# Kernel optimization log

Measured on AMD Instinct MI355X. Metric: run time of the kernel, lower is better.

The kernel has to match this reference:

```python
import jax, jax.numpy as jnp
import numpy as np


def setup_inputs() -> dict:
    key = jax.random.key(0)
    k1, k2 = jax.random.split(key)
    B, N, S, C = 8, 65536, 4, 8
    psi = jax.random.normal(k1, (B, N, S), dtype=jnp.float32)
    # nn.Parameter(torch.randn(d_coord, d_spinor, d_spinor) / sqrt(d_spinor))
    gamma = jax.random.normal(k2, (C, S, S), dtype=jnp.float32) / jnp.sqrt(jnp.float32(S))
    return {"psi": psi, "gamma": gamma}


def reference(psi, gamma):
    # G[mu,nu] = gamma[mu] @ gamma[nu]  -> [C, C, S, S]
    G = jnp.einsum('mij,njk->mnik', gamma, gamma)
    Gt = jnp.swapaxes(G, 0, 1)                 # G[nu,mu]
    A = 0.5 * (G - Gt)                         # 0.5 * commutator  (K1 generator)
    Ssym = 0.5 * (G + Gt)                      # 0.5 * anticommutator (K2 generator)

    # K0: sigma = psi_bar psi (psi_bar == psi here)
    K0 = jnp.einsum('bni,bni->bn', psi, psi)   # [B, N]

    # Precompute small outer product per token, then contract once per output.
    outer = jnp.einsum('bni,bnj->bnij', psi, psi)   # [B, N, S, S] (small S=4)
    K1 = jnp.einsum('bnij,mnuv->bnmn'.replace('nu', 'x'), outer, A) if False else \
         jnp.einsum('bnij,cdij->bncd', outer, A)    # [B, N, C, C] antisymmetric
    K2 = jnp.einsum('bnij,cdij->bncd', outer, Ssym) # [B, N, C, C] symmetric
    return (K0, K1, K2)
```

## Files before the change

kernel.cpp:

```cpp
#include <hip/hip_runtime.h>


#define TPB 128
#define LDS_STRIDE 68

__device__ __forceinline__ float dot4(float4 a, float4 b) {
    return a.x * b.x + a.y * b.y + a.z * b.z + a.w * b.w;
}

__global__ __launch_bounds__(TPB) void spinor_bilinears_kernel(
    const float* __restrict__ psi,
    const float* __restrict__ gamma,
    float* __restrict__ out,
    long long n_tokens) {
    __shared__ float ldsT[TPB * LDS_STRIDE];

    const int tid = threadIdx.x;
    const long long t_glob = (long long)blockIdx.x * TPB + tid;

    float* K0 = out;
    float* K1 = out + n_tokens;
    float* K2 = out + n_tokens + n_tokens * 64;

    const float4 p = ((const float4*)psi)[t_glob];

    K0[t_glob] = dot4(p, p);

    float4 u[8], v[8];
    const float4* g4 = (const float4*)gamma;
#pragma unroll
    for (int c = 0; c < 8; ++c) {
        const float4 g0 = g4[c * 4 + 0];
        const float4 g1 = g4[c * 4 + 1];
        const float4 g2 = g4[c * 4 + 2];
        const float4 g3 = g4[c * 4 + 3];
        float4 uc;
        uc.x = p.x * g0.x + p.y * g1.x + p.z * g2.x + p.w * g3.x;
        uc.y = p.x * g0.y + p.y * g1.y + p.z * g2.y + p.w * g3.y;
        uc.z = p.x * g0.z + p.y * g1.z + p.z * g2.z + p.w * g3.z;
        uc.w = p.x * g0.w + p.y * g1.w + p.z * g2.w + p.w * g3.w;
        u[c] = uc;
        float4 vc;
        vc.x = dot4(g0, p);
        vc.y = dot4(g1, p);
        vc.z = dot4(g2, p);
        vc.w = dot4(g3, p);
        v[c] = vc;
    }

    float* row = &ldsT[tid * LDS_STRIDE];
#pragma unroll
    for (int c = 0; c < 8; ++c) {
        float4 t0, t1;
        t0.x = dot4(u[c], v[0]);
        t0.y = dot4(u[c], v[1]);
        t0.z = dot4(u[c], v[2]);
        t0.w = dot4(u[c], v[3]);
        t1.x = dot4(u[c], v[4]);
        t1.y = dot4(u[c], v[5]);
        t1.z = dot4(u[c], v[6]);
        t1.w = dot4(u[c], v[7]);
        ((float4*)(row + c * 8))[0] = t0;
        ((float4*)(row + c * 8))[1] = t1;
    }

    __syncthreads();

    const long long blk_base = (long long)blockIdx.x * (TPB * 64);
    float4* K1v = (float4*)(K1 + blk_base);
    float4* K2v = (float4*)(K2 + blk_base);

    const int cd0 = (tid & 15) * 4;
    const int c = cd0 >> 3;
    const int d0 = cd0 & 7;

#pragma unroll
    for (int it = 0; it < 16; ++it) {
        const int t = it * 8 + (tid >> 4);
        const float* trow = &ldsT[t * LDS_STRIDE];
        const float4 tcd = *(const float4*)(trow + cd0);
        const float td0 = trow[(d0 + 0) * 8 + c];
        const float td1 = trow[(d0 + 1) * 8 + c];
        const float td2 = trow[(d0 + 2) * 8 + c];
        const float td3 = trow[(d0 + 3) * 8 + c];

        float4 k1v, k2v;
        k1v.x = 0.5f * (tcd.x - td0);  k2v.x = 0.5f * (tcd.x + td0);
        k1v.y = 0.5f * (tcd.y - td1);  k2v.y = 0.5f * (tcd.y + td1);
        k1v.z = 0.5f * (tcd.z - td2);  k2v.z = 0.5f * (tcd.z + td2);
        k1v.w = 0.5f * (tcd.w - td3);  k2v.w = 0.5f * (tcd.w + td3);

        K1v[it * 128 + tid] = k1v;
        K2v[it * 128 + tid] = k2v;
    }
}

extern "C" void kernel_launch(void* const* d_in, const int* in_sizes, int n_in,
                              void* d_out, int out_size, void* d_ws, size_t ws_size,
                              hipStream_t stream) {
    const float* psi = (const float*)d_in[0];
    const float* gamma = (const float*)d_in[1];
    float* out = (float*)d_out;

    const long long n_tokens = (long long)in_sizes[0] / 4;
    const int blocks = (int)(n_tokens / TPB);

    spinor_bilinears_kernel<<<blocks, TPB, 0, stream>>>(psi, gamma, out, n_tokens);
}
```

Before: 269.6 us.

## Assign sixteen threads per token and compute outputs directly without LDS transpose

Replaces the one-thread-per-token kernel, which staged a 64-entry matrix per token through LDS, with a kernel where 16 threads cooperate on a token. Each thread computes one float4 of K1 and K2 directly, recomputing the transposed term instead of reading it from shared memory. This removes the large LDS allocation and barrier, raising occupancy and giving coalesced vector stores, now issued as nontemporal writes. The cost is redundant per-thread arithmetic and repeated gamma loads.

```diff
diff --git a/kernel.cpp b/kernel.cpp
--- a/kernel.cpp
+++ b/kernel.cpp
@@ -1,98 +1,84 @@
 #include <hip/hip_runtime.h>
 
 
-#define TPB 128
-#define LDS_STRIDE 68
+#define TPB 256
+
+typedef float f32x4 __attribute__((ext_vector_type(4)));
 
 __device__ __forceinline__ float dot4(float4 a, float4 b) {
     return a.x * b.x + a.y * b.y + a.z * b.z + a.w * b.w;
 }
 
-__global__ __launch_bounds__(TPB) void spinor_bilinears_kernel(
+__global__ __launch_bounds__(TPB) void spinor_bilinears_direct(
     const float* __restrict__ psi,
     const float* __restrict__ gamma,
     float* __restrict__ out,
     long long n_tokens) {
-    __shared__ float ldsT[TPB * LDS_STRIDE];
+    const long long tau = (long long)blockIdx.x * TPB + threadIdx.x;
+    const long long token = tau >> 4;
+    const int q = (int)(tau & 15);
+    const int c = q >> 1;
+    const int d0 = (q & 1) * 4;
 
-    const int tid = threadIdx.x;
-    const long long t_glob = (long long)blockIdx.x * TPB + tid;
+    const float4* __restrict__ psi4 = (const float4*)psi;
+    const float4* __restrict__ g4 = (const float4*)gamma;
 
     float* K0 = out;
-    float* K1 = out + n_tokens;
-    float* K2 = out + n_tokens + n_tokens * 64;
+    f32x4* K1 = (f32x4*)(out + n_tokens);
+    f32x4* K2 = (f32x4*)(out + n_tokens + n_tokens * 64);
 
-    const float4 p = ((const float4*)psi)[t_glob];
-
-    K0[t_glob] = dot4(p, p);
-
-    float4 u[8], v[8];
-    const float4* g4 = (const float4*)gamma;
-#pragma unroll
-    for (int c = 0; c < 8; ++c) {
-        const float4 g0 = g4[c * 4 + 0];
-        const float4 g1 = g4[c * 4 + 1];
-        const float4 g2 = g4[c * 4 + 2];
-        const float4 g3 = g4[c * 4 + 3];
-        float4 uc;
-        uc.x = p.x * g0.x + p.y * g1.x + p.z * g2.x + p.w * g3.x;
-        uc.y = p.x * g0.y + p.y * g1.y + p.z * g2.y + p.w * g3.y;
-        uc.z = p.x * g0.z + p.y * g1.z + p.z * g2.z + p.w * g3.z;
-        uc.w = p.x * g0.w + p.y * g1.w + p.z * g2.w + p.w * g3.w;
-        u[c] = uc;
-        float4 vc;
-        vc.x = dot4(g0, p);
-        vc.y = dot4(g1, p);
-        vc.z = dot4(g2, p);
-        vc.w = dot4(g3, p);
-        v[c] = vc;
+    if (tau < n_tokens) {
+        const float4 pp = psi4[tau];
+        __builtin_nontemporal_store(dot4(pp, pp), &out[tau]);
     }
 
-    float* row = &ldsT[tid * LDS_STRIDE];
+    const float4 p = psi4[token];
+
+    const float4 gc0 = g4[c * 4 + 0];
+    const float4 gc1 = g4[c * 4 + 1];
+    const float4 gc2 = g4[c * 4 + 2];
+    const float4 gc3 = g4[c * 4 + 3];
+
+    float4 u, w;
+    u.x = p.x * gc0.x + p.y * gc1.x + p.z * gc2.x + p.w * gc3.x;
+    u.y = p.x * gc0.y + p.y * gc1.y + p.z * gc2.y + p.w * gc3.y;
+    u.z = p.x * gc0.z + p.y * gc1.z + p.z * gc2.z + p.w * gc3.z;
+    u.w = p.x * gc0.w + p.y * gc1.w + p.z * gc2.w + p.w * gc3.w;
+    w.x = dot4(gc0, p);
+    w.y = dot4(gc1, p);
+    w.z = dot4(gc2, p);
+    w.w = dot4(gc3, p);
+
+    float k1a[4], k2a[4];
 #pragma unroll
-    for (int c = 0; c < 8; ++c) {
-        float4 t0, t1;
-        t0.x = dot4(u[c], v[0]);
-        t0.y = dot4(u[c], v[1]);
-        t0.z = dot4(u[c], v[2]);
-        t0.w = dot4(u[c], v[3]);
-        t1.x = dot4(u[c], v[4]);
-        t1.y = dot4(u[c], v[5]);
-        t1.z = dot4(u[c], v[6]);
-        t1.w = dot4(u[c], v[7]);
-        ((float4*)(row + c * 8))[0] = t0;
-        ((float4*)(row + c * 8))[1] = t1;
+    for (int k = 0; k < 4; ++k) {
+        const int d = d0 + k;
+        const float4 gd0 = g4[d * 4 + 0];
+        const float4 gd1 = g4[d * 4 + 1];
+        const float4 gd2 = g4[d * 4 + 2];
+        const float4 gd3 = g4[d * 4 + 3];
+
+        const float a0 = dot4(gd0, p);
+        const float a1 = dot4(gd1, p);
+        const float a2 = dot4(gd2, p);
+        const float a3 = dot4(gd3, p);
+        const float b0 = dot4(gd0, w);
+        const float b1 = dot4(gd1, w);
+        const float b2 = dot4(gd2, w);
+        const float b3 = dot4(gd3, w);
+
+        const float tcd = u.x * a0 + u.y * a1 + u.z * a2 + u.w * a3;
+        const float tdc = p.x * b0 + p.y * b1 + p.z * b2 + p.w * b3;
+
+        k1a[k] = 0.5f * (tcd - tdc);
+        k2a[k] = 0.5f * (tcd + tdc);
     }
 
-    __syncthreads();
-
-    const long long blk_base = (long long)blockIdx.x * (TPB * 64);
-    float4* K1v = (float4*)(K1 + blk_base);
-    float4* K2v = (float4*)(K2 + blk_base);
-
-    const int cd0 = (tid & 15) * 4;
-    const int c = cd0 >> 3;
-    const int d0 = cd0 & 7;
-
-#pragma unroll
-    for (int it = 0; it < 16; ++it) {
-        const int t = it * 8 + (tid >> 4);
-        const float* trow = &ldsT[t * LDS_STRIDE];
-        const float4 tcd = *(const float4*)(trow + cd0);
-        const float td0 = trow[(d0 + 0) * 8 + c];
-        const float td1 = trow[(d0 + 1) * 8 + c];
-        const float td2 = trow[(d0 + 2) * 8 + c];
-        const float td3 = trow[(d0 + 3) * 8 + c];
-
-        float4 k1v, k2v;
-        k1v.x = 0.5f * (tcd.x - td0);  k2v.x = 0.5f * (tcd.x + td0);
-        k1v.y = 0.5f * (tcd.y - td1);  k2v.y = 0.5f * (tcd.y + td1);
-        k1v.z = 0.5f * (tcd.z - td2);  k2v.z = 0.5f * (tcd.z + td2);
-        k1v.w = 0.5f * (tcd.w - td3);  k2v.w = 0.5f * (tcd.w + td3);
-
-        K1v[it * 128 + tid] = k1v;
-        K2v[it * 128 + tid] = k2v;
-    }
+    f32x4 o1, o2;
+    o1.x = k1a[0]; o1.y = k1a[1]; o1.z = k1a[2]; o1.w = k1a[3];
+    o2.x = k2a[0]; o2.y = k2a[1]; o2.z = k2a[2]; o2.w = k2a[3];
+    __builtin_nontemporal_store(o1, &K1[tau]);
+    __builtin_nontemporal_store(o2, &K2[tau]);
 }
 
 extern "C" void kernel_launch(void* const* d_in, const int* in_sizes, int n_in,
@@ -103,7 +89,8 @@
     float* out = (float*)d_out;
 
     const long long n_tokens = (long long)in_sizes[0] / 4;
-    const int blocks = (int)(n_tokens / TPB);
+    const long long n_threads = n_tokens * 16;
+    const int blocks = (int)(n_threads / TPB);
 
-    spinor_bilinears_kernel<<<blocks, TPB, 0, stream>>>(psi, gamma, out, n_tokens);
+    spinor_bilinears_direct<<<blocks, TPB, 0, stream>>>(psi, gamma, out, n_tokens);
 }
```

Measured after the change: 368.8 us. +36.8%, slower.
